# Optimization experiments

Hardware: AMD Instinct MI355X
Metric: run time of the kernel (lower is better)

The kernel has to match this reference:

```python
import jax, jax.numpy as jnp
import numpy as np

B, S, HID = 4, 512, 768
NH, HD = 12, 64          # num_heads, head_size = HID // NH
REL = 64                 # rel_dim
NEG_INF = -1e9


def setup_inputs() -> dict:
    key = jax.random.key(0)
    ks = jax.random.split(key, 12)
    input_tensor = jax.random.normal(ks[0], (B, S, HID), jnp.float32)
    graph_matrix = (jax.random.uniform(ks[1], (B, S, S)) < 0.3).astype(jnp.float32)
    # end_mask: one-hot at the last position (null attention slot)
    end_mask = jnp.zeros((B, S), jnp.float32).at[:, S - 1].set(1.0)
    rel_embeddings = jax.random.normal(ks[2], (B, S, S, REL), jnp.float32)
    w = lambda k, shp: jax.random.normal(k, shp, jnp.float32) * 0.02
    return {
        "input_tensor": input_tensor,
        "graph_matrix": graph_matrix,
        "end_mask": end_mask,
        "rel_embeddings": rel_embeddings,
        "Wq": w(ks[3], (HID, HID)), "bq": jnp.zeros((HID,), jnp.float32),
        "Wk": w(ks[4], (HID, HID)), "bk": jnp.zeros((HID,), jnp.float32),
        "Wv": w(ks[5], (HID, HID)), "bv": jnp.zeros((HID,), jnp.float32),
        "Wr": w(ks[6], (REL, HD)), "br": jnp.zeros((HD,), jnp.float32),
    }


def reference(input_tensor, graph_matrix, end_mask, rel_embeddings,
              Wq, bq, Wk, bk, Wv, bv, Wr, br):
    # use_null_att_pos: allow attending to the end/null slot
    g = graph_matrix + end_mask[:, None, :]              # (B,S,S)
    neg_inf_mask = (1.0 - g) * NEG_INF                   # (B,S,S)

    def heads(x):  # (B,S,HID) -> (B,NH,S,HD)
        return x.reshape(B, S, NH, HD).transpose(0, 2, 1, 3)

    q = heads(input_tensor @ Wq + bq)
    k = heads(input_tensor @ Wk + bk)
    v = heads(input_tensor @ Wv + bv)

    rel = rel_embeddings @ Wr + br                       # (B,S,S,HD), shared over heads
    # matmul_rel: (x_i * (y_j + z_ij)).sum(-1) = q.k^T + q.rel, per head
    scores = (jnp.einsum('bhid,bhjd->bhij', q, k)
              + jnp.einsum('bhid,bijd->bhij', q, rel))   # (B,NH,S,S)
    scores = scores / jnp.sqrt(jnp.float32(HD)) + neg_inf_mask[:, None]
    probs = jax.nn.softmax(scores, axis=-1)              # dropout p=0 -> identity

    ctx = jnp.einsum('bhij,bhjd->bhid', probs, v)        # (B,NH,S,HD)
    return ctx.transpose(0, 2, 1, 3).reshape(B, S, NH * HD)
```

## Files before the change

kernel.cpp:

```cpp
#include <hip/hip_runtime.h>
#include <hip/hip_bf16.h>
#include <hip/hip_fp16.h>
#include <cstddef>
#include <cstdint>

typedef __attribute__((ext_vector_type(8))) short bf16x8;
typedef __attribute__((ext_vector_type(4))) float f32x4;

#define MFMA16(a, b, c) __builtin_amdgcn_mfma_f32_16x16x32_bf16((a), (b), (c), 0, 0, 0)

static constexpr int B = 4, S = 512, HID = 768, NH = 12, HD = 64;
static constexpr int QKV_N = B * NH * S * HD;
static constexpr size_t SCORES_N = (size_t)B * NH * S * S;

__device__ __forceinline__ short f2bf(float f) {
  unsigned u = __builtin_bit_cast(unsigned, f);
  u += 0x7FFFu + ((u >> 16) & 1u);
  return (short)(u >> 16);
}
__device__ __forceinline__ float bf2f(short s) {
  unsigned u = ((unsigned)(unsigned short)s) << 16;
  return __builtin_bit_cast(float, u);
}
__device__ __forceinline__ bf16x8 ld_cvt8(const float* __restrict__ p) {
  float4 a = *reinterpret_cast<const float4*>(p);
  float4 b = *reinterpret_cast<const float4*>(p + 4);
  bf16x8 r;
  r[0] = f2bf(a.x); r[1] = f2bf(a.y); r[2] = f2bf(a.z); r[3] = f2bf(a.w);
  r[4] = f2bf(b.x); r[5] = f2bf(b.y); r[6] = f2bf(b.z); r[7] = f2bf(b.w);
  return r;
}
__device__ __forceinline__ f32x4 ld4nt(const float* p) {
  return __builtin_nontemporal_load(reinterpret_cast<const f32x4*>(p));
}
__device__ __forceinline__ bf16x8 cvt8(f32x4 a, f32x4 b) {
  bf16x8 r;
  r[0] = f2bf(a[0]); r[1] = f2bf(a[1]); r[2] = f2bf(a[2]); r[3] = f2bf(a[3]);
  r[4] = f2bf(b[0]); r[5] = f2bf(b[1]); r[6] = f2bf(b[2]); r[7] = f2bf(b[3]);
  return r;
}

__global__ __launch_bounds__(256) void k_qkv(
    const float* __restrict__ x,
    const float* __restrict__ Wq, const float* __restrict__ bq,
    const float* __restrict__ Wk, const float* __restrict__ bk,
    const float* __restrict__ Wv, const float* __restrict__ bv,
    short* __restrict__ qkv) {
  __shared__ short As[64 * 40];
  __shared__ short Bs[64 * 40];
  const int m0 = blockIdx.x * 64;
  const int nt = blockIdx.y;
  const int mat = nt / 12;
  const int nc0 = (nt % 12) * 64;
  const float* __restrict__ W    = (mat == 0) ? Wq : (mat == 1) ? Wk : Wv;
  const float* __restrict__ bias = (mat == 0) ? bq : (mat == 1) ? bk : bv;
  short* __restrict__ outp = qkv + (size_t)mat * QKV_N;
  const int t = threadIdx.x;
  const int w = t >> 6, lane = t & 63;
  const int wm = (w >> 1) * 32, wn = (w & 1) * 32;
  const int lr = lane & 15, lk = lane >> 4;
  f32x4 acc[2][2] = {};
  for (int kk = 0; kk < 768; kk += 32) {
#pragma unroll
    for (int it = 0; it < 2; ++it) {
      int f = it * 256 + t;
      {
        int r = f >> 3, c4 = f & 7;
        float4 v = *reinterpret_cast<const float4*>(x + (size_t)(m0 + r) * 768 + kk + c4 * 4);
        short* d = &As[r * 40 + c4 * 4];
        d[0] = f2bf(v.x); d[1] = f2bf(v.y); d[2] = f2bf(v.z); d[3] = f2bf(v.w);
      }
      {
        int kr = f >> 4, c4 = f & 15;
        float4 v = *reinterpret_cast<const float4*>(W + (size_t)(kk + kr) * 768 + nc0 + c4 * 4);
        int c = c4 * 4;
        Bs[(c + 0) * 40 + kr] = f2bf(v.x);
        Bs[(c + 1) * 40 + kr] = f2bf(v.y);
        Bs[(c + 2) * 40 + kr] = f2bf(v.z);
        Bs[(c + 3) * 40 + kr] = f2bf(v.w);
      }
    }
    __syncthreads();
    bf16x8 a0 = *reinterpret_cast<const bf16x8*>(&As[(wm + lr) * 40 + lk * 8]);
    bf16x8 a1 = *reinterpret_cast<const bf16x8*>(&As[(wm + 16 + lr) * 40 + lk * 8]);
    bf16x8 b0 = *reinterpret_cast<const bf16x8*>(&Bs[(wn + lr) * 40 + lk * 8]);
    bf16x8 b1 = *reinterpret_cast<const bf16x8*>(&Bs[(wn + 16 + lr) * 40 + lk * 8]);
    acc[0][0] = MFMA16(a0, b0, acc[0][0]);
    acc[0][1] = MFMA16(a0, b1, acc[0][1]);
    acc[1][0] = MFMA16(a1, b0, acc[1][0]);
    acc[1][1] = MFMA16(a1, b1, acc[1][1]);
    __syncthreads();
  }
#pragma unroll
  for (int mf = 0; mf < 2; ++mf)
#pragma unroll
    for (int nf = 0; nf < 2; ++nf) {
      int col = nc0 + wn + nf * 16 + lr;
      float bv_ = bias[col];
      int h = col >> 6, d = col & 63;
#pragma unroll
      for (int reg = 0; reg < 4; ++reg) {
        int m = m0 + wm + mf * 16 + lk * 4 + reg;
        int b_ = m >> 9, i = m & 511;
        outp[(size_t)((b_ * NH + h) * S + i) * HD + d] = f2bf(acc[mf][nf][reg] + bv_);
      }
    }
}

__global__ __launch_bounds__(256) void k_qr(const short* __restrict__ q,
                                            const float* __restrict__ Wr,
                                            short* __restrict__ qr) {
  const int i0 = blockIdx.x * 64;
  const int h = blockIdx.y, b = blockIdx.z;
  const short* __restrict__ qp = q + (size_t)((b * NH + h) * S) * HD;
  short* __restrict__ op = qr + (size_t)((b * NH + h) * S) * HD;
  const int t = threadIdx.x;
  const int w = t >> 6, lane = t & 63;
  const int wm = (w >> 1) * 32, wn = (w & 1) * 32;
  const int lr = lane & 15, lk = lane >> 4;
  f32x4 acc[2][2] = {};
#pragma unroll
  for (int ks = 0; ks < 2; ++ks) {
    int k0 = ks * 32 + lk * 8;
    bf16x8 a0 = *reinterpret_cast<const bf16x8*>(qp + (size_t)(i0 + wm + lr) * 64 + k0);
    bf16x8 a1 = *reinterpret_cast<const bf16x8*>(qp + (size_t)(i0 + wm + 16 + lr) * 64 + k0);
    bf16x8 b0 = ld_cvt8(Wr + (size_t)(wn + lr) * 64 + k0);
    bf16x8 b1 = ld_cvt8(Wr + (size_t)(wn + 16 + lr) * 64 + k0);
    acc[0][0] = MFMA16(a0, b0, acc[0][0]);
    acc[0][1] = MFMA16(a0, b1, acc[0][1]);
    acc[1][0] = MFMA16(a1, b0, acc[1][0]);
    acc[1][1] = MFMA16(a1, b1, acc[1][1]);
  }
#pragma unroll
  for (int mf = 0; mf < 2; ++mf)
#pragma unroll
    for (int nf = 0; nf < 2; ++nf) {
      int r = wn + nf * 16 + lr;
#pragma unroll
      for (int reg = 0; reg < 4; ++reg) {
        int i = i0 + wm + mf * 16 + lk * 4 + reg;
        op[(size_t)i * 64 + r] = f2bf(acc[mf][nf][reg] * 0.125f);
      }
    }
}

__global__ __launch_bounds__(256) void k_qk(const short* __restrict__ q,
                                            const short* __restrict__ kmat,
                                            const float* __restrict__ graph,
                                            const float* __restrict__ endm,
                                            __half* __restrict__ sc) {
  const int j0 = blockIdx.x * 64, i0 = blockIdx.y * 64;
  const int bh = blockIdx.z;
  const int b = bh / NH, hh = bh % NH;
  const short* __restrict__ qp = q + (size_t)(bh * S) * HD;
  const short* __restrict__ kp = kmat + (size_t)(bh * S) * HD;
  const int t = threadIdx.x;
  const int w = t >> 6, lane = t & 63;
  const int wm = (w >> 1) * 32, wn = (w & 1) * 32;
  const int lr = lane & 15, lk = lane >> 4;
  f32x4 acc[2][2] = {};
#pragma unroll
  for (int ks = 0; ks < 2; ++ks) {
    int k0 = ks * 32 + lk * 8;
    bf16x8 a0 = *reinterpret_cast<const bf16x8*>(qp + (size_t)(i0 + wm + lr) * 64 + k0);
    bf16x8 a1 = *reinterpret_cast<const bf16x8*>(qp + (size_t)(i0 + wm + 16 + lr) * 64 + k0);
    bf16x8 b0 = *reinterpret_cast<const bf16x8*>(kp + (size_t)(j0 + wn + lr) * 64 + k0);
    bf16x8 b1 = *reinterpret_cast<const bf16x8*>(kp + (size_t)(j0 + wn + 16 + lr) * 64 + k0);
    acc[0][0] = MFMA16(a0, b0, acc[0][0]);
    acc[0][1] = MFMA16(a0, b1, acc[0][1]);
    acc[1][0] = MFMA16(a1, b0, acc[1][0]);
    acc[1][1] = MFMA16(a1, b1, acc[1][1]);
  }
#pragma unroll
  for (int mf = 0; mf < 2; ++mf)
#pragma unroll
    for (int nf = 0; nf < 2; ++nf) {
      int j = j0 + wn + nf * 16 + lr;
      float e = endm[b * S + j];
#pragma unroll
      for (int reg = 0; reg < 4; ++reg) {
        int i = i0 + wm + mf * 16 + lk * 4 + reg;
        float g = graph[(size_t)(b * S + i) * S + j];
        float s = acc[mf][nf][reg] * 0.125f + (1.0f - g - e) * (-30000.0f);
        sc[(((size_t)b * S + i) * NH + hh) * S + j] = __float2half(s);
      }
    }
}

__global__ __launch_bounds__(256) void k_relsm(const short* __restrict__ qrb,
                                               const float* __restrict__ rel,
                                               const __half* __restrict__ sc,
                                               short* __restrict__ probs) {
  __shared__ float den_lds[64];
  const int i = blockIdx.x, b = blockIdx.y;
  const int t = threadIdx.x;
  const int w = t >> 6, lane = t & 63;
  const int lr = lane & 15, fq = lane >> 4;
  const int hA = (lr < NH) ? lr : 0;
  const short* qrow = qrb + ((size_t)(b * NH + hA) * S + i) * 64;
  bf16x8 a0 = *reinterpret_cast<const bf16x8*>(qrow + fq * 8);
  bf16x8 a1 = *reinterpret_cast<const bf16x8*>(qrow + 32 + fq * 8);
  const float* rp = rel + (((size_t)(b * S) + i) * S + (size_t)(w * 128 + lr)) * 64 + fq * 8;
  const __half* scp = sc + ((size_t)(b * S) + i) * NH * S;
  float p[8][4];
  float den[4] = {0.f, 0.f, 0.f, 0.f};
  f32x4 c0 = ld4nt(rp), c1 = ld4nt(rp + 4), c2 = ld4nt(rp + 32), c3 = ld4nt(rp + 36);
#pragma unroll
  for (int tt = 0; tt < 8; ++tt) {
    f32x4 n0, n1, n2, n3;
    if (tt < 7) {
      const float* rn = rp + (size_t)(tt + 1) * 1024;
      n0 = ld4nt(rn); n1 = ld4nt(rn + 4); n2 = ld4nt(rn + 32); n3 = ld4nt(rn + 36);
    }
    bf16x8 b0 = cvt8(c0, c1), b1 = cvt8(c2, c3);
    f32x4 acc = {};
    acc = MFMA16(a0, b0, acc);
    acc = MFMA16(a1, b1, acc);
    const int j0 = w * 128 + tt * 16;
#pragma unroll
    for (int r = 0; r < 4; ++r) {
      int h = fq * 4 + r;
      float s = acc[r] + __half2float(scp[h * S + j0 + lr]);
      float pe = __expf(fminf(s, 80.0f));
      den[r] += pe;
      p[tt][r] = pe;
    }
    if (tt < 7) { c0 = n0; c1 = n1; c2 = n2; c3 = n3; }
  }
#pragma unroll
  for (int r = 0; r < 4; ++r) {
    float d = den[r];
    d += __shfl_xor(d, 1); d += __shfl_xor(d, 2);
    d += __shfl_xor(d, 4); d += __shfl_xor(d, 8);
    den[r] = d;
  }
  if (lr == 0) {
#pragma unroll
    for (int r = 0; r < 4; ++r) den_lds[w * 16 + fq * 4 + r] = den[r];
  }
  __syncthreads();
  float invd[4];
#pragma unroll
  for (int r = 0; r < 4; ++r) {
    int h = fq * 4 + r;
    invd[r] = 1.0f / (den_lds[h] + den_lds[16 + h] + den_lds[32 + h] + den_lds[48 + h]);
  }
#pragma unroll
  for (int tt = 0; tt < 8; ++tt) {
    int j0 = w * 128 + tt * 16;
#pragma unroll
    for (int r = 0; r < 4; ++r) {
      int h = fq * 4 + r;
      if (h < NH)
        probs[((size_t)(b * NH + h) * S + i) * S + j0 + lr] = f2bf(p[tt][r] * invd[r]);
    }
  }
}

__global__ __launch_bounds__(256) void k_pv2(const short* __restrict__ probs,
                                             const short* __restrict__ v,
                                             float* __restrict__ out) {
  __shared__ short vt[64 * 72];
  const int i0 = blockIdx.x * 64;
  const int h = blockIdx.y, b = blockIdx.z;
  const short* __restrict__ vp = v + (size_t)((b * NH + h) * S) * HD;
  const short* __restrict__ pp = probs + (size_t)((b * NH + h) * S) * S;
  const int t = threadIdx.x;
  const int w = t >> 6, lane = t & 63;
  const int wm = (w >> 1) * 32, wn = (w & 1) * 32;
  const int lr = lane & 15, lk = lane >> 4;
  f32x4 acc[2][2] = {};
  for (int j0 = 0; j0 < S; j0 += 64) {
    __syncthreads();
#pragma unroll
    for (int it = 0; it < 2; ++it) {
      int jr = it * 32 + (t >> 3), c8 = t & 7;
      bf16x8 vv = *reinterpret_cast<const bf16x8*>(vp + (size_t)(j0 + jr) * 64 + c8 * 8);
      int jsw = (((jr >> 3) ^ c8) << 3) | (jr & 7);
#pragma unroll
      for (int u = 0; u < 8; ++u) vt[(c8 * 8 + u) * 72 + jsw] = vv[u];
    }
    __syncthreads();
#pragma unroll
    for (int ks = 0; ks < 2; ++ks) {
      const short* prow = pp + j0 + ks * 32 + lk * 8;
      bf16x8 a0 = *reinterpret_cast<const bf16x8*>(prow + (size_t)(i0 + wm + lr) * S);
      bf16x8 a1 = *reinterpret_cast<const bf16x8*>(prow + (size_t)(i0 + wm + 16 + lr) * S);
      int r0 = wn + lr, r1 = wn + 16 + lr;
      int jb = ks * 4 + lk;
      bf16x8 b0 = *reinterpret_cast<const bf16x8*>(&vt[r0 * 72 + ((jb ^ ((r0 >> 3) & 7)) << 3)]);
      bf16x8 b1 = *reinterpret_cast<const bf16x8*>(&vt[r1 * 72 + ((jb ^ ((r1 >> 3) & 7)) << 3)]);
      acc[0][0] = MFMA16(a0, b0, acc[0][0]);
      acc[0][1] = MFMA16(a0, b1, acc[0][1]);
      acc[1][0] = MFMA16(a1, b0, acc[1][0]);
      acc[1][1] = MFMA16(a1, b1, acc[1][1]);
    }
  }
#pragma unroll
  for (int mf = 0; mf < 2; ++mf)
#pragma unroll
    for (int nf = 0; nf < 2; ++nf) {
      int d = wn + nf * 16 + lr;
#pragma unroll
      for (int reg = 0; reg < 4; ++reg) {
        int i = i0 + wm + mf * 16 + lk * 4 + reg;
        out[((size_t)(b * S) + i) * HID + h * 64 + d] = acc[mf][nf][reg];
      }
    }
}

extern "C" void kernel_launch(void* const* d_in, const int* in_sizes, int n_in,
                              void* d_out, int out_size, void* d_ws, size_t ws_size,
                              hipStream_t stream) {
  const float* x     = (const float*)d_in[0];
  const float* graph = (const float*)d_in[1];
  const float* endm  = (const float*)d_in[2];
  const float* rel   = (const float*)d_in[3];
  const float* Wq = (const float*)d_in[4];  const float* bq = (const float*)d_in[5];
  const float* Wk = (const float*)d_in[6];  const float* bk = (const float*)d_in[7];
  const float* Wv = (const float*)d_in[8];  const float* bv = (const float*)d_in[9];
  const float* Wr = (const float*)d_in[10];

  short* qb  = (short*)d_ws;
  short* kb  = qb + QKV_N;
  short* vb  = kb + QKV_N;
  short* qrb = vb + QKV_N;
  __half* scores = (__half*)(qrb + QKV_N);
  short* probs   = (short*)(scores + SCORES_N);
  const size_t need = (size_t)4 * QKV_N * 2 + SCORES_N * 2 + SCORES_N * 2;
  if (ws_size < need) return;

  k_qkv<<<dim3(32, 36), 256, 0, stream>>>(x, Wq, bq, Wk, bk, Wv, bv, qb);
  k_qr<<<dim3(8, NH, B), 256, 0, stream>>>(qb, Wr, qrb);
  k_qk<<<dim3(8, 8, B * NH), 256, 0, stream>>>(qb, kb, graph, endm, scores);
  k_relsm<<<dim3(S, B), 256, 0, stream>>>(qrb, rel, scores, probs);
  k_pv2<<<dim3(8, NH, B), 256, 0, stream>>>(probs, vb, (float*)d_out);
}
```

Before: 162.4 us.

## Fuse q·Wr into QKV GEMM, emit transposed V, stage scores in LDS

The q·Wr projection is folded into the QKV projection kernel, so the separate k_qr launch and its re-read of q are gone. V is now written in transposed layout, which lets the PV kernel load B fragments straight from global memory without an LDS transpose or barriers. The PV grid uses smaller 32-row tiles to get more blocks. The rel/softmax kernel stages each row's fp16 scores for all heads into LDS up front, trading an extra barrier for coalesced loads. Writing transposed V uses strided scalar stores, which may be less efficient.

```diff
diff --git a/kernel.cpp b/kernel.cpp
--- a/kernel.cpp
+++ b/kernel.cpp
@@ -18,9 +18,9 @@
   u += 0x7FFFu + ((u >> 16) & 1u);
   return (short)(u >> 16);
 }
-__device__ __forceinline__ float bf2f(short s) {
-  unsigned u = ((unsigned)(unsigned short)s) << 16;
-  return __builtin_bit_cast(float, u);
+__device__ __forceinline__ float h2f(short s) {
+  __half h = __builtin_bit_cast(__half, (unsigned short)s);
+  return __half2float(h);
 }
 __device__ __forceinline__ bf16x8 ld_cvt8(const float* __restrict__ p) {
   float4 a = *reinterpret_cast<const float4*>(p);
@@ -45,9 +45,11 @@
     const float* __restrict__ Wq, const float* __restrict__ bq,
     const float* __restrict__ Wk, const float* __restrict__ bk,
     const float* __restrict__ Wv, const float* __restrict__ bv,
-    short* __restrict__ qkv) {
+    const float* __restrict__ Wr,
+    short* __restrict__ qkv, short* __restrict__ qrb, short* __restrict__ vT) {
   __shared__ short As[64 * 40];
   __shared__ short Bs[64 * 40];
+  __shared__ short qs[64 * 72];
   const int m0 = blockIdx.x * 64;
   const int nt = blockIdx.y;
   const int mat = nt / 12;
@@ -91,6 +93,23 @@
     acc[1][1] = MFMA16(a1, b1, acc[1][1]);
     __syncthreads();
   }
+  const int b_ = m0 >> 9;
+  if (mat == 2) {
+#pragma unroll
+    for (int mf = 0; mf < 2; ++mf)
+#pragma unroll
+      for (int nf = 0; nf < 2; ++nf) {
+        int col = nc0 + wn + nf * 16 + lr;
+        float bv_ = bias[col];
+        int h = col >> 6, d = col & 63;
+#pragma unroll
+        for (int reg = 0; reg < 4; ++reg) {
+          int j = (m0 + wm + mf * 16 + lk * 4 + reg) & 511;
+          vT[((size_t)(b_ * NH + h) * HD + d) * S + j] = f2bf(acc[mf][nf][reg] + bv_);
+        }
+      }
+    return;
+  }
 #pragma unroll
   for (int mf = 0; mf < 2; ++mf)
 #pragma unroll
@@ -100,48 +119,41 @@
       int h = col >> 6, d = col & 63;
 #pragma unroll
       for (int reg = 0; reg < 4; ++reg) {
-        int m = m0 + wm + mf * 16 + lk * 4 + reg;
-        int b_ = m >> 9, i = m & 511;
-        outp[(size_t)((b_ * NH + h) * S + i) * HD + d] = f2bf(acc[mf][nf][reg] + bv_);
-      }
-    }
-}
-
-__global__ __launch_bounds__(256) void k_qr(const short* __restrict__ q,
-                                            const float* __restrict__ Wr,
-                                            short* __restrict__ qr) {
-  const int i0 = blockIdx.x * 64;
-  const int h = blockIdx.y, b = blockIdx.z;
-  const short* __restrict__ qp = q + (size_t)((b * NH + h) * S) * HD;
-  short* __restrict__ op = qr + (size_t)((b * NH + h) * S) * HD;
-  const int t = threadIdx.x;
-  const int w = t >> 6, lane = t & 63;
-  const int wm = (w >> 1) * 32, wn = (w & 1) * 32;
-  const int lr = lane & 15, lk = lane >> 4;
-  f32x4 acc[2][2] = {};
-#pragma unroll
-  for (int ks = 0; ks < 2; ++ks) {
-    int k0 = ks * 32 + lk * 8;
-    bf16x8 a0 = *reinterpret_cast<const bf16x8*>(qp + (size_t)(i0 + wm + lr) * 64 + k0);
-    bf16x8 a1 = *reinterpret_cast<const bf16x8*>(qp + (size_t)(i0 + wm + 16 + lr) * 64 + k0);
-    bf16x8 b0 = ld_cvt8(Wr + (size_t)(wn + lr) * 64 + k0);
-    bf16x8 b1 = ld_cvt8(Wr + (size_t)(wn + 16 + lr) * 64 + k0);
-    acc[0][0] = MFMA16(a0, b0, acc[0][0]);
-    acc[0][1] = MFMA16(a0, b1, acc[0][1]);
-    acc[1][0] = MFMA16(a1, b0, acc[1][0]);
-    acc[1][1] = MFMA16(a1, b1, acc[1][1]);
-  }
-#pragma unroll
-  for (int mf = 0; mf < 2; ++mf)
-#pragma unroll
-    for (int nf = 0; nf < 2; ++nf) {
-      int r = wn + nf * 16 + lr;
-#pragma unroll
-      for (int reg = 0; reg < 4; ++reg) {
-        int i = i0 + wm + mf * 16 + lk * 4 + reg;
-        op[(size_t)i * 64 + r] = f2bf(acc[mf][nf][reg] * 0.125f);
-      }
-    }
+        int mloc = wm + mf * 16 + lk * 4 + reg;
+        int i = (m0 + mloc) & 511;
+        short qv = f2bf(acc[mf][nf][reg] + bv_);
+        outp[(size_t)((b_ * NH + h) * S + i) * HD + d] = qv;
+        if (mat == 0) qs[mloc * 72 + d] = qv;
+      }
+    }
+  if (mat == 0) {
+    const int h0 = nc0 >> 6;
+    __syncthreads();
+    f32x4 qacc[2][2] = {};
+#pragma unroll
+    for (int ks = 0; ks < 2; ++ks) {
+      int k0 = ks * 32 + lk * 8;
+      bf16x8 a0 = *reinterpret_cast<const bf16x8*>(&qs[(wm + lr) * 72 + k0]);
+      bf16x8 a1 = *reinterpret_cast<const bf16x8*>(&qs[(wm + 16 + lr) * 72 + k0]);
+      bf16x8 b0 = ld_cvt8(Wr + (size_t)(wn + lr) * 64 + k0);
+      bf16x8 b1 = ld_cvt8(Wr + (size_t)(wn + 16 + lr) * 64 + k0);
+      qacc[0][0] = MFMA16(a0, b0, qacc[0][0]);
+      qacc[0][1] = MFMA16(a0, b1, qacc[0][1]);
+      qacc[1][0] = MFMA16(a1, b0, qacc[1][0]);
+      qacc[1][1] = MFMA16(a1, b1, qacc[1][1]);
+    }
+#pragma unroll
+    for (int mf = 0; mf < 2; ++mf)
+#pragma unroll
+      for (int nf = 0; nf < 2; ++nf) {
+        int r = wn + nf * 16 + lr;
+#pragma unroll
+        for (int reg = 0; reg < 4; ++reg) {
+          int i = (m0 + wm + mf * 16 + lk * 4 + reg) & 511;
+          qrb[((size_t)(b_ * NH + h0) * S + i) * 64 + r] = f2bf(qacc[mf][nf][reg] * 0.125f);
+        }
+      }
+  }
 }
 
 __global__ __launch_bounds__(256) void k_qk(const short* __restrict__ q,
@@ -191,20 +203,30 @@
                                                const float* __restrict__ rel,
                                                const __half* __restrict__ sc,
                                                short* __restrict__ probs) {
+  __shared__ short sq[16 * 520];
   __shared__ float den_lds[64];
   const int i = blockIdx.x, b = blockIdx.y;
   const int t = threadIdx.x;
   const int w = t >> 6, lane = t & 63;
   const int lr = lane & 15, fq = lane >> 4;
+  {
+    const short* src = reinterpret_cast<const short*>(sc + ((size_t)(b * S) + i) * NH * S);
+    int hh = t >> 4, js = (t & 15) * 32;
+    const short* sp = src + (size_t)hh * S + js;
+    short* dp = &sq[hh * 520 + js];
+#pragma unroll
+    for (int c = 0; c < 4; ++c)
+      *reinterpret_cast<bf16x8*>(dp + c * 8) = *reinterpret_cast<const bf16x8*>(sp + c * 8);
+  }
   const int hA = (lr < NH) ? lr : 0;
   const short* qrow = qrb + ((size_t)(b * NH + hA) * S + i) * 64;
   bf16x8 a0 = *reinterpret_cast<const bf16x8*>(qrow + fq * 8);
   bf16x8 a1 = *reinterpret_cast<const bf16x8*>(qrow + 32 + fq * 8);
   const float* rp = rel + (((size_t)(b * S) + i) * S + (size_t)(w * 128 + lr)) * 64 + fq * 8;
-  const __half* scp = sc + ((size_t)(b * S) + i) * NH * S;
   float p[8][4];
   float den[4] = {0.f, 0.f, 0.f, 0.f};
   f32x4 c0 = ld4nt(rp), c1 = ld4nt(rp + 4), c2 = ld4nt(rp + 32), c3 = ld4nt(rp + 36);
+  __syncthreads();
 #pragma unroll
   for (int tt = 0; tt < 8; ++tt) {
     f32x4 n0, n1, n2, n3;
@@ -220,7 +242,7 @@
 #pragma unroll
     for (int r = 0; r < 4; ++r) {
       int h = fq * 4 + r;
-      float s = acc[r] + __half2float(scp[h * S + j0 + lr]);
+      float s = acc[r] + h2f(sq[h * 520 + j0 + lr]);
       float pe = __expf(fminf(s, 80.0f));
       den[r] += pe;
       p[tt][r] = pe;
@@ -258,55 +280,38 @@
 }
 
 __global__ __launch_bounds__(256) void k_pv2(const short* __restrict__ probs,
-                                             const short* __restrict__ v,
+                                             const short* __restrict__ vT,
                                              float* __restrict__ out) {
-  __shared__ short vt[64 * 72];
-  const int i0 = blockIdx.x * 64;
+  const int i0 = blockIdx.x * 32;
   const int h = blockIdx.y, b = blockIdx.z;
-  const short* __restrict__ vp = v + (size_t)((b * NH + h) * S) * HD;
-  const short* __restrict__ pp = probs + (size_t)((b * NH + h) * S) * S;
+  const short* __restrict__ pp  = probs + (size_t)((b * NH + h) * S) * S;
+  const short* __restrict__ vtp = vT + (size_t)((b * NH + h) * HD) * S;
   const int t = threadIdx.x;
   const int w = t >> 6, lane = t & 63;
-  const int wm = (w >> 1) * 32, wn = (w & 1) * 32;
+  const int wm = (w >> 1) * 16, wn = (w & 1) * 32;
   const int lr = lane & 15, lk = lane >> 4;
-  f32x4 acc[2][2] = {};
+  f32x4 acc[2] = {};
+#pragma unroll
   for (int j0 = 0; j0 < S; j0 += 64) {
-    __syncthreads();
-#pragma unroll
-    for (int it = 0; it < 2; ++it) {
-      int jr = it * 32 + (t >> 3), c8 = t & 7;
-      bf16x8 vv = *reinterpret_cast<const bf16x8*>(vp + (size_t)(j0 + jr) * 64 + c8 * 8);
-      int jsw = (((jr >> 3) ^ c8) << 3) | (jr & 7);
-#pragma unroll
-      for (int u = 0; u < 8; ++u) vt[(c8 * 8 + u) * 72 + jsw] = vv[u];
-    }
-    __syncthreads();
 #pragma unroll
     for (int ks = 0; ks < 2; ++ks) {
-      const short* prow = pp + j0 + ks * 32 + lk * 8;
-      bf16x8 a0 = *reinterpret_cast<const bf16x8*>(prow + (size_t)(i0 + wm + lr) * S);
-      bf16x8 a1 = *reinterpret_cast<const bf16x8*>(prow + (size_t)(i0 + wm + 16 + lr) * S);
-      int r0 = wn + lr, r1 = wn + 16 + lr;
-      int jb = ks * 4 + lk;
-      bf16x8 b0 = *reinterpret_cast<const bf16x8*>(&vt[r0 * 72 + ((jb ^ ((r0 >> 3) & 7)) << 3)]);
-      bf16x8 b1 = *reinterpret_cast<const bf16x8*>(&vt[r1 * 72 + ((jb ^ ((r1 >> 3) & 7)) << 3)]);
-      acc[0][0] = MFMA16(a0, b0, acc[0][0]);
-      acc[0][1] = MFMA16(a0, b1, acc[0][1]);
-      acc[1][0] = MFMA16(a1, b0, acc[1][0]);
-      acc[1][1] = MFMA16(a1, b1, acc[1][1]);
-    }
-  }
-#pragma unroll
-  for (int mf = 0; mf < 2; ++mf)
-#pragma unroll
-    for (int nf = 0; nf < 2; ++nf) {
-      int d = wn + nf * 16 + lr;
-#pragma unroll
-      for (int reg = 0; reg < 4; ++reg) {
-        int i = i0 + wm + mf * 16 + lk * 4 + reg;
-        out[((size_t)(b * S) + i) * HID + h * 64 + d] = acc[mf][nf][reg];
-      }
-    }
+      int k0 = j0 + ks * 32 + lk * 8;
+      bf16x8 a0 = *reinterpret_cast<const bf16x8*>(pp + (size_t)(i0 + wm + lr) * S + k0);
+      bf16x8 b0 = *reinterpret_cast<const bf16x8*>(vtp + (size_t)(wn + lr) * S + k0);
+      bf16x8 b1 = *reinterpret_cast<const bf16x8*>(vtp + (size_t)(wn + 16 + lr) * S + k0);
+      acc[0] = MFMA16(a0, b0, acc[0]);
+      acc[1] = MFMA16(a0, b1, acc[1]);
+    }
+  }
+#pragma unroll
+  for (int nf = 0; nf < 2; ++nf) {
+    int d = wn + nf * 16 + lr;
+#pragma unroll
+    for (int reg = 0; reg < 4; ++reg) {
+      int i = i0 + wm + lk * 4 + reg;
+      out[((size_t)(b * S) + i) * HID + h * 64 + d] = acc[nf][reg];
+    }
+  }
 }
 
 extern "C" void kernel_launch(void* const* d_in, const int* in_sizes, int n_in,
@@ -323,16 +328,15 @@
 
   short* qb  = (short*)d_ws;
   short* kb  = qb + QKV_N;
-  short* vb  = kb + QKV_N;
-  short* qrb = vb + QKV_N;
+  short* vTb = kb + QKV_N;
+  short* qrb = vTb + QKV_N;
   __half* scores = (__half*)(qrb + QKV_N);
   short* probs   = (short*)(scores + SCORES_N);
   const size_t need = (size_t)4 * QKV_N * 2 + SCORES_N * 2 + SCORES_N * 2;
   if (ws_size < need) return;
 
-  k_qkv<<<dim3(32, 36), 256, 0, stream>>>(x, Wq, bq, Wk, bk, Wv, bv, qb);
-  k_qr<<<dim3(8, NH, B), 256, 0, stream>>>(qb, Wr, qrb);
+  k_qkv<<<dim3(32, 36), 256, 0, stream>>>(x, Wq, bq, Wk, bk, Wv, bv, Wr, qb, qrb, vTb);
   k_qk<<<dim3(8, 8, B * NH), 256, 0, stream>>>(qb, kb, graph, endm, scores);
   k_relsm<<<dim3(S, B), 256, 0, stream>>>(qrb, rel, scores, probs);
-  k_pv2<<<dim3(8, NH, B), 256, 0, stream>>>(probs, vb, (float*)d_out);
-}
+  k_pv2<<<dim3(16, NH, B), 256, 0, stream>>>(probs, vTb, (float*)d_out);
+}
```

After: 164.6 us. Within noise of the previous version (+1.4%).
